# Performance work log

Hardware: AMD Instinct MI355X
Metric: run time of the kernel (lower is better)

## Reference

```python
import jax, jax.numpy as jnp
import numpy as np

ALPHA = 0.1  # init kwarg alpha


def setup_inputs() -> dict:
    key = jax.random.key(0)
    k1, k2 = jax.random.split(key)
    x = jax.random.normal(k1, (32, 192, 64, 64), dtype=jnp.float32)
    delta = jax.random.normal(k2, (32, 1, 64, 64), dtype=jnp.float32)
    return {"x_bchw": x, "delta": delta}


def reference(x_bchw, delta):
    # Faithful fixed-shape version of LayerTokenPrune.forward.
    # Kept tokens are stream-compacted to the front (stable, preserving
    # original token order, matching torch.where index order); dropped
    # positions are zero-padded, matching the zero-pad in the original.
    B, C, H, W = x_bchw.shape
    L = H * W
    tok = jnp.transpose(x_bchw, (0, 2, 3, 1)).reshape(B, L, C)  # [B, L, C]

    delta_tok = delta.reshape(B, -1)  # 4-dim delta branch -> [B, L]
    imp = jnp.abs(delta_tok)
    lo = imp.min(axis=1, keepdims=True)
    hi = imp.max(axis=1, keepdims=True)
    rng = jnp.maximum(hi - lo, 1e-3)  # clamp_min(0.001)
    imp = (imp - lo) / rng

    mu = imp.mean(axis=1, keepdims=True)
    sigma = imp.std(axis=1, keepdims=True, ddof=1)  # torch std is unbiased
    theta = mu - ALPHA * sigma
    keep = imp >= theta  # [B, L] bool; max-imp token always kept (theta<=mu<=1)

    # Stable compaction: kept token indices first, in original order.
    # jnp.argsort is stable, so sorting the key (0 for keep, 1 for drop)
    # reproduces torch.where's ascending-index order for kept tokens.
    order = jnp.argsort(jnp.logical_not(keep).astype(jnp.int32), axis=1)  # [B, L]
    gathered = jnp.take_along_axis(tok, order[:, :, None], axis=1)  # [B, L, C]

    counts = keep.sum(axis=1)  # [B]
    valid = (jnp.arange(L)[None, :] < counts[:, None]).astype(tok.dtype)  # [B, L]
    tok_new = gathered * valid[:, :, None]  # zero out pad positions

    # Fixed-shape analogue of the sqrt reshape: pad to full L = H*W grid.
    y = tok_new.reshape(B, H, W, C).transpose(0, 3, 1, 2)  # [B, C, H, W]

    keep_ratio = counts.astype(jnp.float32).mean() / L
    theta_mean = theta.mean()
    return y, keep_ratio, theta_mean
```

## Files before the change

### kernel.cpp

```cpp
#include <hip/hip_runtime.h>
#include <hip/hip_bf16.h>
#include <math.h>

#define B_ 32
#define C_ 192
#define H_ 64
#define W_ 64
#define L_ 4096
#define L4_ 1024
#define NTHREADS 256
#define PER_THREAD 16

#define SWIZ(i) ((((i) & 3) << 10) | ((i) >> 2))

__global__ __launch_bounds__(NTHREADS) void stats_scan_kernel(
    const float* __restrict__ delta,
    int*  __restrict__ src_idx,
    int*  __restrict__ counts,
    float* __restrict__ thetas)
{
  const int b = blockIdx.x;
  const int t = threadIdx.x;
  const int lane = t & 63;
  const int wid  = t >> 6;

  __shared__ float  smin[4], smax[4];
  __shared__ float  s_lo, s_rng, s_theta;
  __shared__ double dsum[4], dsum2[4];
  __shared__ int    wsum[4];

  const float* dp = delta + (size_t)b * L_;

  float a[PER_THREAD];
  const float4* d4 = (const float4*)dp;
  #pragma unroll
  for (int i = 0; i < 4; ++i) {
    float4 v = d4[t * 4 + i];
    a[i*4+0] = fabsf(v.x); a[i*4+1] = fabsf(v.y);
    a[i*4+2] = fabsf(v.z); a[i*4+3] = fabsf(v.w);
  }

  float lmin = a[0], lmax = a[0];
  #pragma unroll
  for (int i = 1; i < PER_THREAD; ++i) {
    lmin = fminf(lmin, a[i]);
    lmax = fmaxf(lmax, a[i]);
  }
  #pragma unroll
  for (int off = 32; off; off >>= 1) {
    lmin = fminf(lmin, __shfl_down(lmin, off, 64));
    lmax = fmaxf(lmax, __shfl_down(lmax, off, 64));
  }
  if (lane == 0) { smin[wid] = lmin; smax[wid] = lmax; }
  __syncthreads();
  if (t == 0) {
    float lo = fminf(fminf(smin[0], smin[1]), fminf(smin[2], smin[3]));
    float hi = fmaxf(fmaxf(smax[0], smax[1]), fmaxf(smax[2], smax[3]));
    s_lo  = lo;
    s_rng = fmaxf(hi - lo, 1e-3f);
  }
  __syncthreads();
  const float lo  = s_lo;
  const float rng = s_rng;

  double s = 0.0, s2 = 0.0;
  #pragma unroll
  for (int i = 0; i < PER_THREAD; ++i) {
    float imp = (a[i] - lo) / rng;
    a[i] = imp;
    s  += (double)imp;
    s2 += (double)imp * (double)imp;
  }
  #pragma unroll
  for (int off = 32; off; off >>= 1) {
    s  += __shfl_down(s,  off, 64);
    s2 += __shfl_down(s2, off, 64);
  }
  if (lane == 0) { dsum[wid] = s; dsum2[wid] = s2; }
  __syncthreads();
  if (t == 0) {
    double S  = dsum[0]  + dsum[1]  + dsum[2]  + dsum[3];
    double S2 = dsum2[0] + dsum2[1] + dsum2[2] + dsum2[3];
    double mu  = S / (double)L_;
    double var = (S2 - S * S / (double)L_) / (double)(L_ - 1);
    if (var < 0.0) var = 0.0;
    double sigma = sqrt(var);
    s_theta = (float)(mu - 0.1 * sigma);
  }
  __syncthreads();
  const float theta = s_theta;

  int flags = 0, cnt = 0;
  #pragma unroll
  for (int i = 0; i < PER_THREAD; ++i) {
    int k = (a[i] >= theta) ? 1 : 0;
    cnt += k;
    flags |= (k << i);
  }
  int inc = cnt;
  #pragma unroll
  for (int off = 1; off < 64; off <<= 1) {
    int y = __shfl_up(inc, off, 64);
    if (lane >= off) inc += y;
  }
  if (lane == 63) wsum[wid] = inc;
  __syncthreads();
  int base = inc - cnt;
  #pragma unroll
  for (int w = 0; w < 4; ++w)
    if (w < wid) base += wsum[w];

  int* sb = src_idx + (size_t)b * L_;
  int p = base;
  #pragma unroll
  for (int i = 0; i < PER_THREAD; ++i) {
    if ((flags >> i) & 1) { sb[p++] = t * PER_THREAD + i; }
  }
  if (t == NTHREADS - 1) {
    counts[b] = base + cnt;
    thetas[b] = theta;
  }
}

__global__ __launch_bounds__(64) void finalize_kernel(
    const int* __restrict__ counts, const float* __restrict__ thetas,
    float* __restrict__ out_tail)
{
  const int t = threadIdx.x;
  float c  = (t < B_) ? (float)counts[t] : 0.0f;
  float th = (t < B_) ? thetas[t]        : 0.0f;
  #pragma unroll
  for (int off = 32; off; off >>= 1) {
    c  += __shfl_down(c,  off, 64);
    th += __shfl_down(th, off, 64);
  }
  if (t == 0) {
    out_tail[0] = (c / (float)B_) / (float)L_;
    out_tail[1] = th / (float)B_;
  }
}

__global__ __launch_bounds__(NTHREADS) void gather_kernel(
    const float* __restrict__ x,
    const int*  __restrict__ src_idx,
    const int*  __restrict__ counts,
    float* __restrict__ out)
{
  __shared__ float row[L_];

  const int bc = blockIdx.x;
  const int b  = bc / C_;
  const int t  = threadIdx.x;

  const float4* x4 = (const float4*)(x + (size_t)bc * L_);

  #pragma unroll
  for (int i = 0; i < 4; ++i) {
    const int j = t + NTHREADS * i;
    float4 v = x4[j];
    row[(0 << 10) | j] = v.x;
    row[(1 << 10) | j] = v.y;
    row[(2 << 10) | j] = v.z;
    row[(3 << 10) | j] = v.w;
  }
  __syncthreads();

  const int  cnt = counts[b];
  const int4* s4b = (const int4*)(src_idx + (size_t)b * L_);
  float4* o4 = (float4*)(out + (size_t)bc * L_);

  #pragma unroll
  for (int i = 0; i < 4; ++i) {
    const int j  = t + NTHREADS * i;
    const int d0 = j * 4;
    const int4 s = s4b[j];
    float4 r;
    r.x = (d0 + 0 < cnt) ? row[SWIZ(s.x)] : 0.0f;
    r.y = (d0 + 1 < cnt) ? row[SWIZ(s.y)] : 0.0f;
    r.z = (d0 + 2 < cnt) ? row[SWIZ(s.z)] : 0.0f;
    r.w = (d0 + 3 < cnt) ? row[SWIZ(s.w)] : 0.0f;
    o4[j] = r;
  }
}

extern "C" void kernel_launch(void* const* d_in, const int* in_sizes, int n_in,
                              void* d_out, int out_size, void* d_ws, size_t ws_size,
                              hipStream_t stream) {
  const float* x     = (const float*)d_in[0];
  const float* delta = (const float*)d_in[1];
  float* out = (float*)d_out;

  int*   src_idx = (int*)d_ws;
  int*   counts  = (int*)((char*)d_ws + (size_t)B_ * L_ * 4);
  float* thetas  = (float*)((char*)d_ws + (size_t)B_ * L_ * 4 + 128);

  const size_t y_elems = (size_t)B_ * C_ * L_;

  stats_scan_kernel<<<B_, NTHREADS, 0, stream>>>(delta, src_idx, counts, thetas);
  finalize_kernel<<<1, 64, 0, stream>>>(counts, thetas, out + y_elems);
  gather_kernel<<<B_ * C_, NTHREADS, 0, stream>>>(x, src_idx, counts, out);
}
```

Baseline: 187.1 us.

## Process several channels per block with double-buffered LDS prefetch in gather

The gather kernel now handles six channels per block instead of one. It loads the source index vector once and reuses it across those channels. It double-buffers channel rows in shared memory, issuing the global load of the next channel before scattering the current one. This amortizes index loads and block launch overhead and overlaps memory latency with LDS gathers. In exchange it uses fewer blocks (1024), more LDS per block (32KB), and more registers, which may lower occupancy on a bandwidth-bound kernel.

```diff
diff --git a/kernel.cpp b/kernel.cpp
--- a/kernel.cpp
+++ b/kernel.cpp
@@ -10,6 +10,7 @@
 #define L4_ 1024
 #define NTHREADS 256
 #define PER_THREAD 16
+#define CPB 6
 
 #define SWIZ(i) ((((i) & 3) << 10) | ((i) >> 2))
 
@@ -146,40 +147,73 @@
     const int*  __restrict__ counts,
     float* __restrict__ out)
 {
-  __shared__ float row[L_];
-
-  const int bc = blockIdx.x;
-  const int b  = bc / C_;
+  __shared__ float buf[2][L_];
+
+  const int gidx = blockIdx.x;
+  const int b  = gidx >> 5;
+  const int c0 = (gidx & 31) * CPB;
   const int t  = threadIdx.x;
 
-  const float4* x4 = (const float4*)(x + (size_t)bc * L_);
-
-  #pragma unroll
-  for (int i = 0; i < 4; ++i) {
-    const int j = t + NTHREADS * i;
-    float4 v = x4[j];
-    row[(0 << 10) | j] = v.x;
-    row[(1 << 10) | j] = v.y;
-    row[(2 << 10) | j] = v.z;
-    row[(3 << 10) | j] = v.w;
-  }
-  __syncthreads();
-
-  const int  cnt = counts[b];
+  const int cnt = counts[b];
+
   const int4* s4b = (const int4*)(src_idx + (size_t)b * L_);
-  float4* o4 = (float4*)(out + (size_t)bc * L_);
-
-  #pragma unroll
-  for (int i = 0; i < 4; ++i) {
-    const int j  = t + NTHREADS * i;
-    const int d0 = j * 4;
-    const int4 s = s4b[j];
-    float4 r;
-    r.x = (d0 + 0 < cnt) ? row[SWIZ(s.x)] : 0.0f;
-    r.y = (d0 + 1 < cnt) ? row[SWIZ(s.y)] : 0.0f;
-    r.z = (d0 + 2 < cnt) ? row[SWIZ(s.z)] : 0.0f;
-    r.w = (d0 + 3 < cnt) ? row[SWIZ(s.w)] : 0.0f;
-    o4[j] = r;
+  int4 s[4];
+  #pragma unroll
+  for (int i = 0; i < 4; ++i) s[i] = s4b[t + NTHREADS * i];
+
+  const float* xrow0 = x   + ((size_t)b * C_ + c0) * L_;
+  float*       orow0 = out + ((size_t)b * C_ + c0) * L_;
+
+  {
+    const float4* x4 = (const float4*)xrow0;
+    #pragma unroll
+    for (int i = 0; i < 4; ++i) {
+      const int j = t + NTHREADS * i;
+      float4 v = x4[j];
+      buf[0][(0 << 10) | j] = v.x;
+      buf[0][(1 << 10) | j] = v.y;
+      buf[0][(2 << 10) | j] = v.z;
+      buf[0][(3 << 10) | j] = v.w;
+    }
+  }
+
+  #pragma unroll
+  for (int k = 0; k < CPB; ++k) {
+    __syncthreads();
+
+    float4 v[4];
+    if (k + 1 < CPB) {
+      const float4* x4 = (const float4*)(xrow0 + (size_t)(k + 1) * L_);
+      #pragma unroll
+      for (int i = 0; i < 4; ++i) v[i] = x4[t + NTHREADS * i];
+    }
+
+    const float* rb = buf[k & 1];
+    float4* o4 = (float4*)(orow0 + (size_t)k * L_);
+    #pragma unroll
+    for (int i = 0; i < 4; ++i) {
+      const int j  = t + NTHREADS * i;
+      const int d0 = j * 4;
+      const int4 si = s[i];
+      float4 r;
+      r.x = (d0 + 0 < cnt) ? rb[SWIZ(si.x)] : 0.0f;
+      r.y = (d0 + 1 < cnt) ? rb[SWIZ(si.y)] : 0.0f;
+      r.z = (d0 + 2 < cnt) ? rb[SWIZ(si.z)] : 0.0f;
+      r.w = (d0 + 3 < cnt) ? rb[SWIZ(si.w)] : 0.0f;
+      o4[j] = r;
+    }
+
+    if (k + 1 < CPB) {
+      float* wb = buf[(k + 1) & 1];
+      #pragma unroll
+      for (int i = 0; i < 4; ++i) {
+        const int j = t + NTHREADS * i;
+        wb[(0 << 10) | j] = v[i].x;
+        wb[(1 << 10) | j] = v[i].y;
+        wb[(2 << 10) | j] = v[i].z;
+        wb[(3 << 10) | j] = v[i].w;
+      }
+    }
   }
 }
 
@@ -198,5 +232,5 @@
 
   stats_scan_kernel<<<B_, NTHREADS, 0, stream>>>(delta, src_idx, counts, thetas);
   finalize_kernel<<<1, 64, 0, stream>>>(counts, thetas, out + y_elems);
-  gather_kernel<<<B_ * C_, NTHREADS, 0, stream>>>(x, src_idx, counts, out);
-}
+  gather_kernel<<<B_ * (C_ / CPB), NTHREADS, 0, stream>>>(x, src_idx, counts, out);
+}
```

Measured after the change: 190.1 us. Within noise of the previous version (+1.6%).
